# Performance work log

Measured on AMD Instinct MI355X. Metric: run time of the kernel, lower is better.

Reference implementation:

```python
import jax, jax.numpy as jnp
import numpy as np

N_NODES = 10240
N_EDGES = 40960
N_GRAPHS = 256
F_XD = 78
SEQ = 1000
VOCAB = 26
EMB = 128
NEG_SLOPE = 0.2


def gat_conv(x, src, dst, W, att_src, att_dst, bias, heads, f_out):
    """PyG GATConv (concat=True, self-loops, leaky_relu 0.2, dst-segment softmax)."""
    N = x.shape[0]
    h = (x @ W).reshape(N, heads, f_out)                      # [N,H,F]
    a_s = jnp.sum(h * att_src[None], axis=-1)                 # [N,H]
    a_d = jnp.sum(h * att_dst[None], axis=-1)                 # [N,H]
    loop = jnp.arange(N, dtype=src.dtype)
    s = jnp.concatenate([src, loop])                          # add self-loops
    d = jnp.concatenate([dst, loop])
    e = jax.nn.leaky_relu(a_s[s] + a_d[d], NEG_SLOPE)         # [E',H]
    m = jax.ops.segment_max(e, d, num_segments=N)             # stable softmax per dst
    e = jnp.exp(e - m[d])
    denom = jax.ops.segment_sum(e, d, num_segments=N)
    alpha = e / (denom[d] + 1e-16)                            # [E',H]
    out = jax.ops.segment_sum(alpha[:, :, None] * h[s], d, num_segments=N)
    return out.reshape(N, heads * f_out) + bias


def conv1d(x, w, b):
    y = jax.lax.conv_general_dilated(x, w, window_strides=(1,), padding='VALID',
                                     dimension_numbers=('NCH', 'OIH', 'NCH'))
    return y + b[None, :, None]


def maxpool1d(x, k):
    return jax.lax.reduce_window(x, -jnp.inf, jax.lax.max, (1, 1, k), (1, 1, k), 'VALID')


def setup_inputs() -> dict:
    key = jax.random.key(0)
    ks = jax.random.split(key, 32)
    x = jax.random.normal(ks[0], (N_NODES, F_XD), jnp.float32)
    src = jax.random.randint(ks[1], (N_EDGES,), 0, N_NODES, dtype=jnp.int32)
    dst = jax.random.randint(ks[2], (N_EDGES,), 0, N_NODES, dtype=jnp.int32)
    dst = jnp.where(dst == src, (dst + 1) % N_NODES, dst)     # no pre-existing self loops
    edge_index = jnp.stack([src, dst])
    batch = jnp.repeat(jnp.arange(N_GRAPHS, dtype=jnp.int32), N_NODES // N_GRAPHS)
    target = jax.random.randint(ks[3], (N_GRAPHS, SEQ), 0, VOCAB, dtype=jnp.int32)
    def w(k, shape):
        return jax.random.normal(k, shape, jnp.float32) * 0.05
    p = {
        'W1': w(ks[4], (78, 10 * 78)), 'as1': w(ks[5], (10, 78)), 'ad1': w(ks[6], (10, 78)), 'b1': jnp.zeros((780,), jnp.float32),
        'W2': w(ks[7], (780, 2 * 780)), 'as2': w(ks[8], (2, 780)), 'ad2': w(ks[9], (2, 780)), 'b2': jnp.zeros((1560,), jnp.float32),
        'W3': w(ks[10], (1560, 3120)), 'as3': w(ks[11], (1, 3120)), 'ad3': w(ks[12], (1, 3120)), 'b3': jnp.zeros((3120,), jnp.float32),
        'fc_g1_w': w(ks[13], (3120, 1024)), 'fc_g1_b': jnp.zeros((1024,), jnp.float32),
        'fc_g2_w': w(ks[14], (1024, 128)), 'fc_g2_b': jnp.zeros((128,), jnp.float32),
        'emb_xt': w(ks[15], (VOCAB, EMB)),
        'cw1': w(ks[16], (32, 1000, 8)), 'cb1': jnp.zeros((32,), jnp.float32),
        'cw2': w(ks[17], (64, 32, 8)), 'cb2': jnp.zeros((64,), jnp.float32),
        'cw3': w(ks[18], (96, 64, 8)), 'cb3': jnp.zeros((96,), jnp.float32),
        'cw4': w(ks[19], (128, 96, 8)), 'cb4': jnp.zeros((128,), jnp.float32),
        'fc1_xt_w': w(ks[20], (128 * 33, 1024)), 'fc1_xt_b': jnp.zeros((1024,), jnp.float32),
        'fc2_xt_w': w(ks[21], (1024, 128)), 'fc2_xt_b': jnp.zeros((128,), jnp.float32),
        'fc1_w': w(ks[22], (256, 1024)), 'fc1_b': jnp.zeros((1024,), jnp.float32),
        'fc2_w': w(ks[23], (1024, 256)), 'fc2_b': jnp.zeros((256,), jnp.float32),
        'out_w': w(ks[24], (256, 1)), 'out_b': jnp.zeros((1,), jnp.float32),
    }
    return {'x': x, 'edge_index': edge_index, 'batch': batch, 'target': target, **p}


def reference(x, edge_index, batch, target,
              W1, as1, ad1, b1, W2, as2, ad2, b2, W3, as3, ad3, b3,
              fc_g1_w, fc_g1_b, fc_g2_w, fc_g2_b, emb_xt,
              cw1, cb1, cw2, cb2, cw3, cb3, cw4, cb4,
              fc1_xt_w, fc1_xt_b, fc2_xt_w, fc2_xt_b,
              fc1_w, fc1_b, fc2_w, fc2_b, out_w, out_b):
    src, dst = edge_index[0], edge_index[1]
    # --- GAT branch (dropout layers are identity in eval mode) ---
    h = jax.nn.elu(gat_conv(x, src, dst, W1, as1, ad1, b1, 10, 78))
    h = jax.nn.relu(gat_conv(h, src, dst, W2, as2, ad2, b2, 2, 780))
    h = jax.nn.relu(gat_conv(h, src, dst, W3, as3, ad3, b3, 1, 3120))
    g = jax.ops.segment_max(h, batch, num_segments=N_GRAPHS)   # global max pool
    g = jax.nn.relu(g @ fc_g1_w + fc_g1_b)
    g = g @ fc_g2_w + fc_g2_b                                  # [B,128]
    # --- protein CNN branch ---
    e = emb_xt[target]                                         # [B,1000,128]
    c = jax.nn.relu(conv1d(e, cw1, cb1))                       # [B,32,121]
    c = jax.nn.relu(conv1d(c, cw2, cb2))                       # [B,64,114]
    c = jax.nn.relu(conv1d(c, cw3, cb3))                       # [B,96,107]
    c = jax.nn.relu(conv1d(c, cw4, cb4))                       # [B,128,100]
    c = maxpool1d(c, 3)                                        # [B,128,33]
    xt = c.reshape(N_GRAPHS, 128 * 33)
    xt = jax.nn.relu(xt @ fc1_xt_w + fc1_xt_b)
    xt = xt @ fc2_xt_w + fc2_xt_b                              # [B,128]
    # --- fusion head ---
    xc = jnp.concatenate([g, xt], axis=1)                      # [B,256]
    xc = jax.nn.relu(xc @ fc1_w + fc1_b)
    xc = jax.nn.relu(xc @ fc2_w + fc2_b)
    return xc @ out_w + out_b                                  # [B,1]
```

## Files before the change

### kernel.cpp

```cpp
#include <hip/hip_runtime.h>
#include <hip/hip_bf16.h>
#include <math.h>

static const int NNODES = 10240;
static const int NEDGES = 40960;
static const int NB     = 256;
static const int VOCAB  = 26;
static const int EMB    = 128;
static const int LP     = 128;
static const int C1SPLIT = 8;

typedef short bf16x8 __attribute__((ext_vector_type(8)));
typedef float f32x4  __attribute__((ext_vector_type(4)));

__device__ __forceinline__ float bf16bits2float(short s) {
    return __uint_as_float(((unsigned)(unsigned short)s) << 16);
}

__global__ __launch_bounds__(256) void gemm_f32_splitk_sl(
    const float* __restrict__ A, const float* __restrict__ B,
    float* __restrict__ P, int M, int N, int K, int kchunk)
{
    __shared__ float As[16][65];
    __shared__ float Bs[16][65];
    int tid = threadIdx.x;
    int bm = blockIdx.y * 64;
    int bn = blockIdx.x * 64;
    int z = blockIdx.z;
    int k0 = z * kchunk;
    int k1 = min(k0 + kchunk, K);
    int tx = tid & 15, ty = tid >> 4;
    float acc[4][4] = {};
    for (int kb = k0; kb < k1; kb += 16) {
#pragma unroll
        for (int l = 0; l < 4; ++l) {
            int idx = tid + l * 256;
            int r = idx >> 4, c = idx & 15;
            int gr = bm + r, gc = kb + c;
            As[c][r] = (gr < M && gc < k1) ? A[(size_t)gr * K + gc] : 0.f;
        }
#pragma unroll
        for (int l = 0; l < 4; ++l) {
            int idx = tid + l * 256;
            int r = idx >> 6, c = idx & 63;
            int gr = kb + r, gc = bn + c;
            Bs[r][c] = (gr < k1 && gc < N) ? B[(size_t)gr * N + gc] : 0.f;
        }
        __syncthreads();
#pragma unroll
        for (int kk = 0; kk < 16; ++kk) {
            float a[4], b[4];
#pragma unroll
            for (int i = 0; i < 4; ++i) a[i] = As[kk][ty * 4 + i];
#pragma unroll
            for (int j = 0; j < 4; ++j) b[j] = Bs[kk][tx * 4 + j];
#pragma unroll
            for (int i = 0; i < 4; ++i)
#pragma unroll
                for (int j = 0; j < 4; ++j)
                    acc[i][j] += a[i] * b[j];
        }
        __syncthreads();
    }
    float* Pz = P + (size_t)z * M * N;
#pragma unroll
    for (int i = 0; i < 4; ++i) {
        int gr = bm + ty * 4 + i;
        if (gr >= M) continue;
#pragma unroll
        for (int j = 0; j < 4; ++j) {
            int gc = bn + tx * 4 + j;
            if (gc >= N) continue;
            Pz[(size_t)gr * N + gc] = acc[i][j];
        }
    }
}

template<int ACT>
__global__ void reduce_bias_act_ld_kernel(const float* __restrict__ P,
                                          const float* __restrict__ bias,
                                          float* __restrict__ C,
                                          int M, int N, int S, int ldC)
{
    int t = blockIdx.x * 256 + threadIdx.x;
    if (t >= M * N) return;
    int r = t / N, c = t - r * N;
    float v = bias[c];
    for (int s = 0; s < S; ++s) v += P[(size_t)s * M * N + t];
    if (ACT == 1) v = fmaxf(v, 0.f);
    C[(size_t)r * ldC + c] = v;
}

__global__ void out_head_kernel(const float* __restrict__ f2,
                                const float* __restrict__ w,
                                const float* __restrict__ b,
                                float* __restrict__ out)
{
    __shared__ float sw[256];
    int t = threadIdx.x;
    sw[t] = w[t];
    __syncthreads();
    float acc = 0.f;
    const float* row = f2 + (size_t)t * 256;
    for (int k = 0; k < 256; ++k) acc += row[k] * sw[k];
    out[t] = acc + b[0];
}

__global__ void cast_a_kernel(const float* __restrict__ in, __hip_bfloat16* __restrict__ out,
                              int M, int K, int Kp)
{
    int idx = blockIdx.x * 256 + threadIdx.x;
    if (idx >= M * Kp) return;
    int r = idx / Kp, k = idx - r * Kp;
    out[idx] = __float2bfloat16(k < K ? in[(size_t)r * K + k] : 0.f);
}

__global__ __launch_bounds__(256) void transpose_cast_kernel(
    const float* __restrict__ in, __hip_bfloat16* __restrict__ out,
    int K, int N, int Kp, int Npad)
{
    __shared__ float tile[32][33];
    int k0 = blockIdx.x * 32;
    int n0 = blockIdx.y * 32;
    int tx = threadIdx.x & 31;
    int ty = threadIdx.x >> 5;
#pragma unroll
    for (int j = 0; j < 4; ++j) {
        int k = k0 + ty + j * 8, n = n0 + tx;
        tile[ty + j * 8][tx] = (k < K && n < N) ? in[(size_t)k * N + n] : 0.f;
    }
    __syncthreads();
#pragma unroll
    for (int j = 0; j < 4; ++j) {
        int n = n0 + ty + j * 8, k = k0 + tx;
        if (n < Npad && k < Kp)
            out[(size_t)n * Kp + k] = __float2bfloat16(tile[tx][ty + j * 8]);
    }
}

__global__ void conv_wt_all_kernel(
    const float* __restrict__ cw2, const float* __restrict__ cw3,
    const float* __restrict__ cw4, const float* __restrict__ cw1,
    __hip_bfloat16* __restrict__ wt2, __hip_bfloat16* __restrict__ wt3,
    __hip_bfloat16* __restrict__ wt4, float* __restrict__ wt1f)
{
    int idx = blockIdx.x * 256 + threadIdx.x;
    const int n2 = 64 * 32 * 8, n3 = 96 * 64 * 8, n4 = 128 * 96 * 8;
    if (idx < n2) {
        int o = idx / (32 * 8), rem = idx - o * 32 * 8;
        int i = rem >> 3, k = rem & 7;
        wt2[(size_t)o * 256 + k * 32 + i] = __float2bfloat16(cw2[idx]);
    } else if (idx < n2 + n3) {
        int j = idx - n2;
        int o = j / (64 * 8), rem = j - o * 64 * 8;
        int i = rem >> 3, k = rem & 7;
        wt3[(size_t)o * 512 + k * 64 + i] = __float2bfloat16(cw3[j]);
    } else if (idx < n2 + n3 + n4) {
        int j = idx - n2 - n3;
        int o = j / (96 * 8), rem = j - o * 96 * 8;
        int i = rem >> 3, k = rem & 7;
        wt4[(size_t)o * 768 + k * 96 + i] = __float2bfloat16(cw4[j]);
    } else {
        int j = idx - n2 - n3 - n4;
        if (j >= 32 * 8000) return;
        int o = j / 8000, rem = j - o * 8000;
        int i = rem >> 3, k = rem & 7;
        wt1f[(size_t)i * 256 + o * 8 + k] = cw1[j];
    }
}

__device__ __forceinline__ void stage_tile(
    const __hip_bfloat16* __restrict__ gA, int ldA,
    const __hip_bfloat16* __restrict__ gB, int ldB,
    short* ldsbuf, int w, int l)
{
#pragma unroll
    for (int j = 0; j < 4; ++j) {
        int u = (w * 4 + j) * 64 + l;
        int r = u >> 3, s = u & 7;
        const __hip_bfloat16* src = gA + (size_t)r * ldA + ((s ^ (r & 7)) << 3);
        __builtin_amdgcn_global_load_lds(
            (const __attribute__((address_space(1))) void*)src,
            (__attribute__((address_space(3))) void*)(ldsbuf + (w * 4 + j) * 512),
            16, 0, 0);
    }
#pragma unroll
    for (int j = 0; j < 4; ++j) {
        int u = (w * 4 + j) * 64 + l;
        int r = u >> 3, s = u & 7;
        const __hip_bfloat16* src = gB + (size_t)r * ldB + ((s ^ (r & 7)) << 3);
        __builtin_amdgcn_global_load_lds(
            (const __attribute__((address_space(1))) void*)src,
            (__attribute__((address_space(3))) void*)(ldsbuf + 8192 + (w * 4 + j) * 512),
            16, 0, 0);
    }
}

__global__ __launch_bounds__(256, 2) void gemm_mfma_bf16(
    const __hip_bfloat16* __restrict__ A,
    const __hip_bfloat16* __restrict__ Bt,
    __hip_bfloat16* __restrict__ C, int M, int N, int Kp, int ldC)
{
    __shared__ __align__(16) short lds[2][16384];
    const int tid = threadIdx.x;
    const int w = tid >> 6, l = tid & 63;

    int nwg = gridDim.x * gridDim.y;
    int wg = blockIdx.y * gridDim.x + blockIdx.x;
    int q = nwg >> 3, r8 = nwg & 7;
    int xcd = wg & 7, lo = wg >> 3;
    int swz = (xcd < r8) ? (xcd * (q + 1) + lo) : (r8 * (q + 1) + (xcd - r8) * q + lo);
    const int bm = (swz / gridDim.x) * 128, bn = (swz % gridDim.x) * 128;

    const int wr = w >> 1, wc = w & 1;
    const int lane15 = l & 15, lhi = l >> 4;

    const __hip_bfloat16* gA = A + (size_t)bm * Kp;
    const __hip_bfloat16* gB = Bt + (size_t)bn * Kp;

    f32x4 acc[4][4] = {};

    const int nk = Kp >> 6;
    stage_tile(gA, Kp, gB, Kp, &lds[0][0], w, l);
    __syncthreads();
    int cur = 0;
    for (int t = 0; t < nk; ++t) {
        if (t + 1 < nk)
            stage_tile(gA + (t + 1) * 64, Kp, gB + (t + 1) * 64, Kp, &lds[cur ^ 1][0], w, l);
        const short* bA = &lds[cur][0];
        const short* bB = &lds[cur][8192];
#pragma unroll
        for (int ks = 0; ks < 2; ++ks) {
            bf16x8 af[4], bfr[4];
#pragma unroll
            for (int m = 0; m < 4; ++m) {
                int r = wr * 64 + m * 16 + lane15;
                int slot = (ks * 4 + lhi) ^ (r & 7);
                af[m] = *(const bf16x8*)(bA + r * 64 + slot * 8);
            }
#pragma unroll
            for (int n = 0; n < 4; ++n) {
                int r = wc * 64 + n * 16 + lane15;
                int slot = (ks * 4 + lhi) ^ (r & 7);
                bfr[n] = *(const bf16x8*)(bB + r * 64 + slot * 8);
            }
#pragma unroll
            for (int m = 0; m < 4; ++m)
#pragma unroll
                for (int n = 0; n < 4; ++n)
                    acc[m][n] = __builtin_amdgcn_mfma_f32_16x16x32_bf16(
                        af[m], bfr[n], acc[m][n], 0, 0, 0);
        }
        __syncthreads();
        cur ^= 1;
    }
#pragma unroll
    for (int m = 0; m < 4; ++m) {
#pragma unroll
        for (int n = 0; n < 4; ++n) {
            int col = bn + wc * 64 + n * 16 + lane15;
            if (col >= N) continue;
            int row0 = bm + wr * 64 + m * 16 + lhi * 4;
#pragma unroll
            for (int q2 = 0; q2 < 4; ++q2)
                C[(size_t)(row0 + q2) * ldC + col] = __float2bfloat16(acc[m][n][q2]);
        }
    }
}

__global__ __launch_bounds__(256, 2) void gemm_mfma_splitk(
    const __hip_bfloat16* __restrict__ A,
    const __hip_bfloat16* __restrict__ Bt,
    float* __restrict__ P, int M, int N, int Kp, int tps)
{
    __shared__ __align__(16) short lds[2][16384];
    const int tid = threadIdx.x;
    const int w = tid >> 6, l = tid & 63;
    const int bm = blockIdx.y * 128, bn = blockIdx.x * 128;
    const int z = blockIdx.z;
    const int wr = w >> 1, wc = w & 1;
    const int lane15 = l & 15, lhi = l >> 4;

    const __hip_bfloat16* gA = A + (size_t)bm * Kp + z * tps * 64;
    const __hip_bfloat16* gB = Bt + (size_t)bn * Kp + z * tps * 64;

    f32x4 acc[4][4] = {};

    const int nk = tps;
    stage_tile(gA, Kp, gB, Kp, &lds[0][0], w, l);
    __syncthreads();
    int cur = 0;
    for (int t = 0; t < nk; ++t) {
        if (t + 1 < nk)
            stage_tile(gA + (t + 1) * 64, Kp, gB + (t + 1) * 64, Kp, &lds[cur ^ 1][0], w, l);
        const short* bA = &lds[cur][0];
        const short* bB = &lds[cur][8192];
#pragma unroll
        for (int ks = 0; ks < 2; ++ks) {
            bf16x8 af[4], bfr[4];
#pragma unroll
            for (int m = 0; m < 4; ++m) {
                int r = wr * 64 + m * 16 + lane15;
                int slot = (ks * 4 + lhi) ^ (r & 7);
                af[m] = *(const bf16x8*)(bA + r * 64 + slot * 8);
            }
#pragma unroll
            for (int n = 0; n < 4; ++n) {
                int r = wc * 64 + n * 16 + lane15;
                int slot = (ks * 4 + lhi) ^ (r & 7);
                bfr[n] = *(const bf16x8*)(bB + r * 64 + slot * 8);
            }
#pragma unroll
            for (int m = 0; m < 4; ++m)
#pragma unroll
                for (int n = 0; n < 4; ++n)
                    acc[m][n] = __builtin_amdgcn_mfma_f32_16x16x32_bf16(
                        af[m], bfr[n], acc[m][n], 0, 0, 0);
        }
        __syncthreads();
        cur ^= 1;
    }
    float* Pz = P + (size_t)z * M * N;
#pragma unroll
    for (int m = 0; m < 4; ++m) {
#pragma unroll
        for (int n = 0; n < 4; ++n) {
            int col = bn + wc * 64 + n * 16 + lane15;
            if (col >= N) continue;
            int row0 = bm + wr * 64 + m * 16 + lhi * 4;
#pragma unroll
            for (int q2 = 0; q2 < 4; ++q2) {
                int row = row0 + q2;
                if (row < M) Pz[(size_t)row * N + col] = acc[m][n][q2];
            }
        }
    }
}

template<int Ci, int Co, int Lout>
__global__ __launch_bounds__(256, 2) void gemm_conv_bf16(
    const __hip_bfloat16* __restrict__ A,
    const __hip_bfloat16* __restrict__ Bt,
    const float* __restrict__ bias,
    __hip_bfloat16* __restrict__ C)
{
    const int Kp = 8 * Ci;
    __shared__ __align__(16) short lds[2][16384];
    const int tid = threadIdx.x;
    const int w = tid >> 6, l = tid & 63;
    const int bm = blockIdx.y * 128;
    const int wr = w >> 1, wc = w & 1;
    const int lane15 = l & 15, lhi = l >> 4;

    const __hip_bfloat16* gA = A + (size_t)bm * Ci;
    const __hip_bfloat16* gB = Bt;

    f32x4 acc[4][4] = {};

    const int nk = Kp >> 6;
    stage_tile(gA, Ci, gB, Kp, &lds[0][0], w, l);
    __syncthreads();
    int cur = 0;
    for (int t = 0; t < nk; ++t) {
        if (t + 1 < nk)
            stage_tile(gA + (t + 1) * 64, Ci, gB + (t + 1) * 64, Kp, &lds[cur ^ 1][0], w, l);
        const short* bA = &lds[cur][0];
        const short* bB = &lds[cur][8192];
#pragma unroll
        for (int ks = 0; ks < 2; ++ks) {
            bf16x8 af[4], bfr[4];
#pragma unroll
            for (int m = 0; m < 4; ++m) {
                int r = wr * 64 + m * 16 + lane15;
                int slot = (ks * 4 + lhi) ^ (r & 7);
                af[m] = *(const bf16x8*)(bA + r * 64 + slot * 8);
            }
#pragma unroll
            for (int n = 0; n < 4; ++n) {
                int r = wc * 64 + n * 16 + lane15;
                int slot = (ks * 4 + lhi) ^ (r & 7);
                bfr[n] = *(const bf16x8*)(bB + r * 64 + slot * 8);
            }
#pragma unroll
            for (int m = 0; m < 4; ++m)
#pragma unroll
                for (int n = 0; n < 4; ++n)
                    acc[m][n] = __builtin_amdgcn_mfma_f32_16x16x32_bf16(
                        af[m], bfr[n], acc[m][n], 0, 0, 0);
        }
        __syncthreads();
        cur ^= 1;
    }
#pragma unroll
    for (int m = 0; m < 4; ++m) {
#pragma unroll
        for (int n = 0; n < 4; ++n) {
            int col = wc * 64 + n * 16 + lane15;
            if (col >= Co) continue;
            float bb = bias[col];
            int lr0 = wr * 64 + m * 16 + lhi * 4;
#pragma unroll
            for (int q2 = 0; q2 < 4; ++q2) {
                int lr = lr0 + q2;
                if (lr < Lout)
                    C[((size_t)bm + lr) * Co + col] =
                        __float2bfloat16(fmaxf(acc[m][n][q2] + bb, 0.f));
            }
        }
    }
}

__global__ __launch_bounds__(256, 2) void gemm_conv4_pool_bf16(
    const __hip_bfloat16* __restrict__ A,
    const __hip_bfloat16* __restrict__ Bt,
    const float* __restrict__ bias,
    __hip_bfloat16* __restrict__ xtb)
{
    const int Ci = 96, Kp = 768;
    __shared__ __align__(16) short lds[2][16384];
    const int tid = threadIdx.x;
    const int w = tid >> 6, l = tid & 63;
    const int bm = blockIdx.y * 128;
    const int wr = w >> 1, wc = w & 1;
    const int lane15 = l & 15, lhi = l >> 4;

    const __hip_bfloat16* gA = A + (size_t)bm * Ci;
    const __hip_bfloat16* gB = Bt;

    f32x4 acc[4][4] = {};

    const int nk = Kp >> 6;
    stage_tile(gA, Ci, gB, Kp, &lds[0][0], w, l);
    __syncthreads();
    int cur = 0;
    for (int t = 0; t < nk; ++t) {
        if (t + 1 < nk)
            stage_tile(gA + (t + 1) * 64, Ci, gB + (t + 1) * 64, Kp, &lds[cur ^ 1][0], w, l);
        const short* bA = &lds[cur][0];
        const short* bB = &lds[cur][8192];
#pragma unroll
        for (int ks = 0; ks < 2; ++ks) {
            bf16x8 af[4], bfr[4];
#pragma unroll
            for (int m = 0; m < 4; ++m) {
                int r = wr * 64 + m * 16 + lane15;
                int slot = (ks * 4 + lhi) ^ (r & 7);
                af[m] = *(const bf16x8*)(bA + r * 64 + slot * 8);
            }
#pragma unroll
            for (int n = 0; n < 4; ++n) {
                int r = wc * 64 + n * 16 + lane15;
                int slot = (ks * 4 + lhi) ^ (r & 7);
                bfr[n] = *(const bf16x8*)(bB + r * 64 + slot * 8);
            }
#pragma unroll
            for (int m = 0; m < 4; ++m)
#pragma unroll
                for (int n = 0; n < 4; ++n)
                    acc[m][n] = __builtin_amdgcn_mfma_f32_16x16x32_bf16(
                        af[m], bfr[n], acc[m][n], 0, 0, 0);
        }
        __syncthreads();
        cur ^= 1;
    }
    float* pbuf = (float*)&lds[0][0];
#pragma unroll
    for (int m = 0; m < 4; ++m) {
#pragma unroll
        for (int n = 0; n < 4; ++n) {
            int col = wc * 64 + n * 16 + lane15;
            float bb = bias[col];
            int lr0 = wr * 64 + m * 16 + lhi * 4;
#pragma unroll
            for (int q2 = 0; q2 < 4; ++q2)
                pbuf[(lr0 + q2) * 128 + col] = acc[m][n][q2] + bb;
        }
    }
    __syncthreads();
    int nb = blockIdx.y;
    for (int idx = tid; idx < 4352; idx += 256) {
        __hip_bfloat16 v;
        if (idx >= 4224) {
            v = __float2bfloat16(0.f);
        } else {
            int c = idx / 33, tp = idx - c * 33;
            float m3 = fmaxf(fmaxf(pbuf[(tp * 3) * 128 + c], pbuf[(tp * 3 + 1) * 128 + c]),
                             pbuf[(tp * 3 + 2) * 128 + c]);
            v = __float2bfloat16(fmaxf(m3, 0.f));
        }
        xtb[(size_t)nb * 4352 + idx] = v;
    }
}

__device__ __forceinline__ unsigned fmap(float f) {
    unsigned u = __float_as_uint(f);
    return (u & 0x80000000u) ? ~u : (u | 0x80000000u);
}
__device__ __forceinline__ float funmap(unsigned u) {
    return (u & 0x80000000u) ? __uint_as_float(u ^ 0x80000000u)
                             : __uint_as_float(~u);
}

__global__ void attn_ab_kernel(const __hip_bfloat16* __restrict__ lin, int Ftp,
                               const float* __restrict__ att_s,
                               const float* __restrict__ att_d,
                               float* __restrict__ a_s, float* __restrict__ a_d,
                               int H, int F)
{
    int bid = blockIdx.x;
    int n = bid / H, h = bid - n * H;
    int lane = threadIdx.x;
    const __hip_bfloat16* row = lin + (size_t)n * Ftp + h * F;
    const float* wsrc = att_s + h * F;
    const float* wdst = att_d + h * F;
    float ss = 0.f, sd = 0.f;
    for (int f = lane; f < F; f += 64) {
        float v = __bfloat162float(row[f]);
        ss += v * wsrc[f];
        sd += v * wdst[f];
    }
    for (int o = 32; o; o >>= 1) {
        ss += __shfl_down(ss, o);
        sd += __shfl_down(sd, o);
    }
    if (lane == 0) { a_s[bid] = ss; a_d[bid] = sd; }
}

__global__ void edge_max_kernel(const int* __restrict__ ei,
                                const float* __restrict__ a_s,
                                const float* __restrict__ a_d,
                                float* __restrict__ eval,
                                unsigned* __restrict__ mmax,
                                int E, int Etot, int H)
{
    int t = blockIdx.x * blockDim.x + threadIdx.x;
    if (t >= Etot * H) return;
    int e = t / H, h = t - e * H;
    int s, d;
    if (e < E) { s = ei[e]; d = ei[E + e]; } else { s = d = e - E; }
    float v = a_s[s * H + h] + a_d[d * H + h];
    v = v > 0.f ? v : 0.2f * v;
    eval[t] = v;
    atomicMax(&mmax[d * H + h], fmap(v));
}

__global__ void edge_exp_kernel(const int* __restrict__ ei,
                                const unsigned* __restrict__ mmax,
                                float* __restrict__ eval,
                                float* __restrict__ denom,
                                int E, int Etot, int H)
{
    int t = blockIdx.x * blockDim.x + threadIdx.x;
    if (t >= Etot * H) return;
    int e = t / H, h = t - e * H;
    int d = (e < E) ? ei[E + e] : e - E;
    float m = funmap(mmax[d * H + h]);
    float ex = expf(eval[t] - m);
    eval[t] = ex;
    atomicAdd(&denom[d * H + h], ex);
}

__global__ void deg_kernel(const int* __restrict__ ei, int* __restrict__ deg,
                           int E, int Etot)
{
    int e = blockIdx.x * 256 + threadIdx.x;
    if (e >= Etot) return;
    int d = (e < E) ? ei[E + e] : e - E;
    atomicAdd(&deg[d], 1);
}

__global__ __launch_bounds__(256) void scan_kernel(const int* __restrict__ deg,
                                                   int* __restrict__ rowptr,
                                                   int* __restrict__ cursor, int n)
{
    __shared__ int partial[256];
    int tid = threadIdx.x;
    const int per = (n + 255) / 256;
    int base = tid * per;
    int sum = 0;
    for (int i = 0; i < per; ++i) {
        int idx = base + i;
        if (idx < n) sum += deg[idx];
    }
    partial[tid] = sum;
    __syncthreads();
    for (int offs = 1; offs < 256; offs <<= 1) {
        int v = (tid >= offs) ? partial[tid - offs] : 0;
        __syncthreads();
        partial[tid] += v;
        __syncthreads();
    }
    int run = (tid == 0) ? 0 : partial[tid - 1];
    for (int i = 0; i < per; ++i) {
        int idx = base + i;
        if (idx < n) { rowptr[idx] = run; cursor[idx] = run; run += deg[idx]; }
    }
    if (tid == 255) rowptr[n] = run;
}

__global__ void fill_csr_kernel(const int* __restrict__ ei, int* __restrict__ cursor,
                                int* __restrict__ eidx, int E, int Etot)
{
    int e = blockIdx.x * 256 + threadIdx.x;
    if (e >= Etot) return;
    int d = (e < E) ? ei[E + e] : e - E;
    int pos = atomicAdd(&cursor[d], 1);
    eidx[pos] = e;
}

template<int ACT>
__global__ __launch_bounds__(64) void gat_gather8_kernel(
    const int* __restrict__ rowptr, const int* __restrict__ eidx,
    const int* __restrict__ ei, const float* __restrict__ eval,
    const float* __restrict__ denom,
    const __hip_bfloat16* __restrict__ lin, int Ftp,
    const float* __restrict__ bias,
    __hip_bfloat16* __restrict__ outh, int Kout,
    int E, int H, int F, int Ft)
{
    int d = blockIdx.x;
    int g = blockIdx.y * 64 + threadIdx.x;
    int c0 = g * 8;
    if (c0 >= Kout) return;
    bf16x8 res;
    if (c0 >= Ft) {
#pragma unroll
        for (int j = 0; j < 8; ++j) res[j] = 0;
        *(bf16x8*)(outh + (size_t)d * Kout + c0) = res;
        return;
    }
    int hj[8];
    float rdh[8];
#pragma unroll
    for (int j = 0; j < 8; ++j) {
        hj[j] = min((c0 + j) / F, H - 1);
        rdh[j] = 1.f / (denom[d * H + hj[j]] + 1e-16f);
    }
    float acc[8] = {};
    int p0 = rowptr[d], p1 = rowptr[d + 1];
    for (int p = p0; p < p1; ++p) {
        int e = eidx[p];
        int s = (e < E) ? ei[e] : e - E;
        bf16x8 v = *(const bf16x8*)(lin + (size_t)s * Ftp + c0);
        const float* aE = eval + (size_t)e * H;
        if (H == 1) {
            float a = aE[0] * rdh[0];
#pragma unroll
            for (int j = 0; j < 8; ++j)
                acc[j] += a * bf16bits2float(v[j]);
        } else {
#pragma unroll
            for (int j = 0; j < 8; ++j)
                acc[j] += aE[hj[j]] * rdh[j] * bf16bits2float(v[j]);
        }
    }
#pragma unroll
    for (int j = 0; j < 8; ++j) {
        int c = c0 + j;
        float val = 0.f;
        if (c < Ft) {
            val = acc[j] + bias[c];
            if (ACT == 1) val = fmaxf(val, 0.f);
            else if (ACT == 2) val = val > 0.f ? val : expm1f(val);
        }
        __hip_bfloat16 bv = __float2bfloat16(val);
        res[j] = *(const short*)&bv;
    }
    *(bf16x8*)(outh + (size_t)d * Kout + c0) = res;
}

__global__ void pool_max_bf16_kernel(const __hip_bfloat16* __restrict__ h,
                                     __hip_bfloat16* __restrict__ g,
                                     int B, int per, int C, int Kout)
{
    int t = blockIdx.x * blockDim.x + threadIdx.x;
    if (t >= B * Kout) return;
    int b = t / Kout, f = t - b * Kout;
    if (f >= C) { g[t] = __float2bfloat16(0.f); return; }
    const __hip_bfloat16* p = h + (size_t)b * per * C + f;
    float m = -INFINITY;
    for (int j = 0; j < per; ++j) m = fmaxf(m, __bfloat162float(p[(size_t)j * C]));
    g[t] = __float2bfloat16(m);
}

__global__ __launch_bounds__(256) void conv1_p1_kernel(
    const int* __restrict__ target, const float* __restrict__ wt,
    float* __restrict__ Spart)
{
    __shared__ float s_S[VOCAB * 256];
    __shared__ int   s_trow[125];
    int tid = threadIdx.x;
    int n = blockIdx.x, z = blockIdx.y;
    for (int i = tid; i < VOCAB * 256; i += 256) s_S[i] = 0.f;
    if (tid < 125) s_trow[tid] = target[n * 1000 + z * 125 + tid];
    __syncthreads();
    const float* wz = wt + (size_t)(z * 125) * 256 + tid;
    for (int i = 0; i < 125; ++i) {
        int v = s_trow[i];
        s_S[v * 256 + tid] += wz[(size_t)i * 256];
    }
    __syncthreads();
    float* outp = Spart + ((size_t)n * C1SPLIT + z) * (VOCAB * 256);
    for (int i = tid; i < VOCAB * 256; i += 256) outp[i] = s_S[i];
}

__global__ __launch_bounds__(256) void conv1_p2_kernel(
    const float* __restrict__ Spart, const float* __restrict__ emb,
    const float* __restrict__ b, __hip_bfloat16* __restrict__ y)
{
    __shared__ float s_emb[VOCAB * EMB];
    __shared__ float s_S[VOCAB * 256];
    int tid = threadIdx.x;
    int n = blockIdx.x;
    for (int i = tid; i < VOCAB * EMB; i += 256) s_emb[i] = emb[i];
    const float* base = Spart + (size_t)n * C1SPLIT * (VOCAB * 256);
    for (int i = tid; i < VOCAB * 256; i += 256) {
        float s = 0.f;
#pragma unroll
        for (int z = 0; z < C1SPLIT; ++z) s += base[(size_t)z * (VOCAB * 256) + i];
        s_S[i] = s;
    }
    __syncthreads();
    for (int idx = tid; idx < 121 * 32; idx += 256) {
        int t = idx >> 5, o = idx & 31;
        float acc = b[o];
#pragma unroll
        for (int v = 0; v < VOCAB; ++v) {
            const float* Sv = s_S + v * 256 + o * 8;
            const float* ev = s_emb + v * EMB + t;
#pragma unroll
            for (int k = 0; k < 8; ++k) acc += Sv[k] * ev[k];
        }
        y[((size_t)n * LP + t) * 32 + o] = __float2bfloat16(fmaxf(acc, 0.f));
    }
}

extern "C" void kernel_launch(void* const* d_in, const int* in_sizes, int n_in,
                              void* d_out, int out_size, void* d_ws, size_t ws_size,
                              hipStream_t stream)
{
    const float* x      = (const float*)d_in[0];
    const int*   ei     = (const int*)d_in[1];
    const int*   target = (const int*)d_in[3];
    const float* W1  = (const float*)d_in[4];
    const float* as1 = (const float*)d_in[5];
    const float* ad1 = (const float*)d_in[6];
    const float* b1  = (const float*)d_in[7];
    const float* W2  = (const float*)d_in[8];
    const float* as2 = (const float*)d_in[9];
    const float* ad2 = (const float*)d_in[10];
    const float* b2  = (const float*)d_in[11];
    const float* W3  = (const float*)d_in[12];
    const float* as3 = (const float*)d_in[13];
    const float* ad3 = (const float*)d_in[14];
    const float* b3  = (const float*)d_in[15];
    const float* fc_g1_w = (const float*)d_in[16];
    const float* fc_g1_b = (const float*)d_in[17];
    const float* fc_g2_w = (const float*)d_in[18];
    const float* fc_g2_b = (const float*)d_in[19];
    const float* emb_xt  = (const float*)d_in[20];
    const float* cw1 = (const float*)d_in[21];
    const float* cb1 = (const float*)d_in[22];
    const float* cw2 = (const float*)d_in[23];
    const float* cb2 = (const float*)d_in[24];
    const float* cw3 = (const float*)d_in[25];
    const float* cb3 = (const float*)d_in[26];
    const float* cw4 = (const float*)d_in[27];
    const float* cb4 = (const float*)d_in[28];
    const float* fc1_xt_w = (const float*)d_in[29];
    const float* fc1_xt_b = (const float*)d_in[30];
    const float* fc2_xt_w = (const float*)d_in[31];
    const float* fc2_xt_b = (const float*)d_in[32];
    const float* fc1_w = (const float*)d_in[33];
    const float* fc1_b = (const float*)d_in[34];
    const float* fc2_w = (const float*)d_in[35];
    const float* fc2_b = (const float*)d_in[36];
    const float* out_w = (const float*)d_in[37];
    const float* out_b = (const float*)d_in[38];
    float* out = (float*)d_out;

    const int N = NNODES, E = NEDGES, Etot = E + N;
    const size_t MB = 1024 * 1024;

    char* ws = (char*)d_ws;
    size_t off = 0;
    auto alloc = [&](size_t bytes) -> char* {
        char* p = ws + off;
        off = (off + bytes + 255) & ~(size_t)255;
        return p;
    };
    const size_t BIG = (size_t)N * 3120 * sizeof(float);
    char*  bufA  = alloc(BIG);
    char*  bufB  = alloc(BIG);
    float*    a_s   = (float*)alloc((size_t)N * 10 * 4);
    float*    a_d   = (float*)alloc((size_t)N * 10 * 4);
    char*     mmdn  = alloc((size_t)2 * N * 10 * 4);
    float*    eval  = (float*)alloc((size_t)Etot * 10 * 4);
    float*    g1    = (float*)alloc((size_t)NB * 1024 * 4);
    float*    xt1   = (float*)alloc((size_t)NB * 1024 * 4);
    float*    xc    = (float*)alloc((size_t)NB * 256 * 4);
    float*    f1    = (float*)alloc((size_t)NB * 1024 * 4);
    float*    f2    = (float*)alloc((size_t)NB * 256 * 4);
    __hip_bfloat16* gbufb = (__hip_bfloat16*)alloc((size_t)NB * 3200 * 2);
    __hip_bfloat16* xtb   = (__hip_bfloat16*)alloc((size_t)NB * 4352 * 2);
    int*      deg     = (int*)alloc((size_t)N * 4);
    int*      rowptr  = (int*)alloc((size_t)(N + 1) * 4);
    int*      cursor  = (int*)alloc((size_t)N * 4);
    int*      eidx    = (int*)alloc((size_t)Etot * 4);

    __hip_bfloat16* linb = (__hip_bfloat16*)bufA;
    __hip_bfloat16* Wt   = (__hip_bfloat16*)(bufA + 64 * MB);
    __hip_bfloat16* xb   = (__hip_bfloat16*)(bufA + 80 * MB);
    __hip_bfloat16* hbf1 = (__hip_bfloat16*)bufB;
    __hip_bfloat16* hbf2 = (__hip_bfloat16*)(bufB + 20 * MB);
    __hip_bfloat16* hbf3 = (__hip_bfloat16*)bufB;
    __hip_bfloat16* Wt2  = (__hip_bfloat16*)(bufB + 105 * MB);
    float*          P4   = (float*)(bufB + 115 * MB);

    char* cnn = bufA;
    auto calloc2 = [&](size_t bytes) -> char* {
        char* p = cnn;
        cnn += (bytes + 255) & ~(size_t)255;
        return p;
    };
    __hip_bfloat16* act1 = (__hip_bfloat16*)calloc2((size_t)NB * LP * 32 * 2 + 4096);
    __hip_bfloat16* act2 = (__hip_bfloat16*)calloc2((size_t)NB * LP * 64 * 2 + 4096);
    __hip_bfloat16* act3 = (__hip_bfloat16*)calloc2((size_t)NB * LP * 96 * 2 + 4096);
    __hip_bfloat16* wt2  = (__hip_bfloat16*)calloc2((size_t)128 * 256 * 2);
    __hip_bfloat16* wt3  = (__hip_bfloat16*)calloc2((size_t)128 * 512 * 2);
    __hip_bfloat16* wt4  = (__hip_bfloat16*)calloc2((size_t)128 * 768 * 2);
    float* wt1f  = (float*)calloc2((size_t)1000 * 256 * 4);
    float* Spart = (float*)calloc2((size_t)NB * C1SPLIT * VOCAB * 256 * 4);

    {
        (void)hipMemsetAsync(deg, 0, (size_t)N * 4, stream);
        deg_kernel<<<(Etot + 255) / 256, 256, 0, stream>>>(ei, deg, E, Etot);
        scan_kernel<<<1, 256, 0, stream>>>(deg, rowptr, cursor, N);
        fill_csr_kernel<<<(Etot + 255) / 256, 256, 0, stream>>>(ei, cursor, eidx, E, Etot);
    }

    auto head_gemm = [&](const float* A, const float* B, const float* bias, float* C,
                         int M, int Nc, int K, int ldC, int act, int S) {
        int kchunk = (K + S - 1) / S;
        dim3 g((Nc + 63) / 64, (M + 63) / 64, S);
        gemm_f32_splitk_sl<<<g, 256, 0, stream>>>(A, B, P4, M, Nc, K, kchunk);
        int tot = M * Nc;
        if (act == 1)
            reduce_bias_act_ld_kernel<1><<<(tot + 255) / 256, 256, 0, stream>>>(P4, bias, C, M, Nc, S, ldC);
        else
            reduce_bias_act_ld_kernel<0><<<(tot + 255) / 256, 256, 0, stream>>>(P4, bias, C, M, Nc, S, ldC);
    };

    auto head_gemm_mfma = [&](const __hip_bfloat16* Ab_, const float* W, const float* bias,
                              float* C, int M, int Nc, int K, int Kp, int S) {
        int tps = (Kp / 64) / S;
        transpose_cast_kernel<<<dim3(Kp / 32, Nc / 32), 256, 0, stream>>>(W, Wt2, K, Nc, Kp, Nc);
        dim3 g(Nc / 128, M / 128, S);
        gemm_mfma_splitk<<<g, 256, 0, stream>>>(Ab_, Wt2, P4, M, Nc, Kp, tps);
        int tot = M * Nc;
        reduce_bias_act_ld_kernel<1><<<(tot + 255) / 256, 256, 0, stream>>>(P4, bias, C, M, Nc, S, Nc);
    };

    auto gat_tail = [&](const float* atts, const float* attd, const float* bias,
                        int H, int F, int Ftp, int act,
                        const __hip_bfloat16* lin, __hip_bfloat16* outh, int Kout) {
        unsigned* mmax = (unsigned*)mmdn;
        float* denom = (float*)(mmdn + (size_t)N * H * 4);
        attn_ab_kernel<<<N * H, 64, 0, stream>>>(lin, Ftp, atts, attd, a_s, a_d, H, F);
        (void)hipMemsetAsync(mmdn, 0, (size_t)2 * N * H * 4, stream);
        int tot = Etot * H;
        edge_max_kernel<<<(tot + 255) / 256, 256, 0, stream>>>(ei, a_s, a_d, eval, mmax, E, Etot, H);
        edge_exp_kernel<<<(tot + 255) / 256, 256, 0, stream>>>(ei, mmax, eval, denom, E, Etot, H);
        int Ft = H * F;
        int groups = Kout / 8;
        dim3 gg(N, (groups + 63) / 64);
        if (act == 1)
            gat_gather8_kernel<1><<<gg, 64, 0, stream>>>(rowptr, eidx, ei, eval, denom, lin, Ftp, bias, outh, Kout, E, H, F, Ft);
        else
            gat_gather8_kernel<2><<<gg, 64, 0, stream>>>(rowptr, eidx, ei, eval, denom, lin, Ftp, bias, outh, Kout, E, H, F, Ft);
    };

    {
        (void)hipMemsetAsync(linb, 0, (size_t)N * 784 * 2, stream);
        cast_a_kernel<<<(N * 128 + 255) / 256, 256, 0, stream>>>(x, xb, N, 78, 128);
        transpose_cast_kernel<<<dim3(4, 28), 256, 0, stream>>>(W1, Wt, 78, 780, 128, 896);
        gemm_mfma_bf16<<<dim3(7, N / 128), 256, 0, stream>>>(xb, Wt, linb, N, 780, 128, 784);
        gat_tail(as1, ad1, b1, 10, 78, 784, 2, linb, hbf1, 832);
    }
    {
        const int Kp = 832, Nout = 1560, Npad = 1664;
        transpose_cast_kernel<<<dim3(Kp / 32, Npad / 32), 256, 0, stream>>>(W2, Wt, 780, Nout, Kp, Npad);
        gemm_mfma_bf16<<<dim3(Npad / 128, N / 128), 256, 0, stream>>>(hbf1, Wt, linb, N, Nout, Kp, Nout);
        gat_tail(as2, ad2, b2, 2, 780, 1560, 1, linb, hbf2, 1600);
    }
    {
        const int Kp = 1600, Nout = 3120, Npad = 3200;
        transpose_cast_kernel<<<dim3(Kp / 32, Npad / 32), 256, 0, stream>>>(W3, Wt, 1560, Nout, Kp, Npad);
        gemm_mfma_bf16<<<dim3(Npad / 128, N / 128), 256, 0, stream>>>(hbf2, Wt, linb, N, Nout, Kp, Nout);
        gat_tail(as3, ad3, b3, 1, 3120, 3120, 1, linb, hbf3, 3120);
    }

    {
        int tot = NB * 3200;
        pool_max_bf16_kernel<<<(tot + 255) / 256, 256, 0, stream>>>(hbf3, gbufb, NB, N / NB, 3120, 3200);
        head_gemm_mfma(gbufb, fc_g1_w, fc_g1_b, g1, NB, 1024, 3120, 3200, 5);
        head_gemm(g1, fc_g2_w, fc_g2_b, xc, NB, 128, 1024, 256, 0, 32);
    }

    {
        conv_wt_all_kernel<<<(64 * 32 * 8 + 96 * 64 * 8 + 128 * 96 * 8 + 32 * 8000 + 255) / 256,
                             256, 0, stream>>>(cw2, cw3, cw4, cw1, wt2, wt3, wt4, wt1f);
        conv1_p1_kernel<<<dim3(NB, C1SPLIT), 256, 0, stream>>>(target, wt1f, Spart);
        conv1_p2_kernel<<<NB, 256, 0, stream>>>(Spart, emb_xt, cb1, act1);
        gemm_conv_bf16<32, 64, 114><<<dim3(1, NB), 256, 0, stream>>>(act1, wt2, cb2, act2);
        gemm_conv_bf16<64, 96, 107><<<dim3(1, NB), 256, 0, stream>>>(act2, wt3, cb3, act3);
        gemm_conv4_pool_bf16<<<dim3(1, NB), 256, 0, stream>>>(act3, wt4, cb4, xtb);
        head_gemm_mfma(xtb, fc1_xt_w, fc1_xt_b, xt1, NB, 1024, 4224, 4352, 4);
        head_gemm(xt1, fc2_xt_w, fc2_xt_b, xc + 128, NB, 128, 1024, 256, 0, 32);
    }

    {
        head_gemm(xc, fc1_w, fc1_b, f1, NB, 1024, 256, 1024, 1, 8);
        head_gemm(f1, fc2_w, fc2_b, f2, NB, 256, 1024, 256, 1, 16);
        out_head_kernel<<<1, 256, 0, stream>>>(f2, out_w, out_b, out);
    }
}
```

Baseline: 793.5 us.

## Fuse GAT edge softmax into CSR gather kernel, dropping atomic max/sum passes

Removes the separate edge_max and edge_exp kernels, the memset and the eval/denominator buffers. Each gather thread now recomputes the leaky-relu attention logits for its destination's incoming edges, takes the per-head max in a first pass, then computes the exp weights, their sum and the weighted feature accumulation in a second pass, normalising at the end. This removes atomics and several launches per layer. In exchange, every column-group thread recomputes the softmax terms redundantly and walks the edge list twice.

```diff
diff --git a/kernel.cpp b/kernel.cpp
--- a/kernel.cpp
+++ b/kernel.cpp
@@ -492,15 +492,6 @@
     }
 }
 
-__device__ __forceinline__ unsigned fmap(float f) {
-    unsigned u = __float_as_uint(f);
-    return (u & 0x80000000u) ? ~u : (u | 0x80000000u);
-}
-__device__ __forceinline__ float funmap(unsigned u) {
-    return (u & 0x80000000u) ? __uint_as_float(u ^ 0x80000000u)
-                             : __uint_as_float(~u);
-}
-
 __global__ void attn_ab_kernel(const __hip_bfloat16* __restrict__ lin, int Ftp,
                                const float* __restrict__ att_s,
                                const float* __restrict__ att_d,
@@ -526,40 +517,6 @@
     if (lane == 0) { a_s[bid] = ss; a_d[bid] = sd; }
 }
 
-__global__ void edge_max_kernel(const int* __restrict__ ei,
-                                const float* __restrict__ a_s,
-                                const float* __restrict__ a_d,
-                                float* __restrict__ eval,
-                                unsigned* __restrict__ mmax,
-                                int E, int Etot, int H)
-{
-    int t = blockIdx.x * blockDim.x + threadIdx.x;
-    if (t >= Etot * H) return;
-    int e = t / H, h = t - e * H;
-    int s, d;
-    if (e < E) { s = ei[e]; d = ei[E + e]; } else { s = d = e - E; }
-    float v = a_s[s * H + h] + a_d[d * H + h];
-    v = v > 0.f ? v : 0.2f * v;
-    eval[t] = v;
-    atomicMax(&mmax[d * H + h], fmap(v));
-}
-
-__global__ void edge_exp_kernel(const int* __restrict__ ei,
-                                const unsigned* __restrict__ mmax,
-                                float* __restrict__ eval,
-                                float* __restrict__ denom,
-                                int E, int Etot, int H)
-{
-    int t = blockIdx.x * blockDim.x + threadIdx.x;
-    if (t >= Etot * H) return;
-    int e = t / H, h = t - e * H;
-    int d = (e < E) ? ei[E + e] : e - E;
-    float m = funmap(mmax[d * H + h]);
-    float ex = expf(eval[t] - m);
-    eval[t] = ex;
-    atomicAdd(&denom[d * H + h], ex);
-}
-
 __global__ void deg_kernel(const int* __restrict__ ei, int* __restrict__ deg,
                            int E, int Etot)
 {
@@ -611,8 +568,8 @@
 template<int ACT>
 __global__ __launch_bounds__(64) void gat_gather8_kernel(
     const int* __restrict__ rowptr, const int* __restrict__ eidx,
-    const int* __restrict__ ei, const float* __restrict__ eval,
-    const float* __restrict__ denom,
+    const int* __restrict__ ei,
+    const float* __restrict__ a_s, const float* __restrict__ a_d,
     const __hip_bfloat16* __restrict__ lin, int Ftp,
     const float* __restrict__ bias,
     __hip_bfloat16* __restrict__ outh, int Kout,
@@ -629,37 +586,62 @@
         *(bf16x8*)(outh + (size_t)d * Kout + c0) = res;
         return;
     }
-    int hj[8];
-    float rdh[8];
-#pragma unroll
-    for (int j = 0; j < 8; ++j) {
-        hj[j] = min((c0 + j) / F, H - 1);
-        rdh[j] = 1.f / (denom[d * H + hj[j]] + 1e-16f);
-    }
-    float acc[8] = {};
+    int h0 = min(c0 / F, H - 1);
+    int h1 = min((c0 + 7) / F, H - 1);
+    int split = (h1 == h0) ? 8 : (F * (h0 + 1) - c0);
+    float ad0 = a_d[d * H + h0];
+    float ad1 = (h1 == h0) ? ad0 : a_d[d * H + h1];
     int p0 = rowptr[d], p1 = rowptr[d + 1];
+
+    float m0 = -INFINITY, m1 = -INFINITY;
     for (int p = p0; p < p1; ++p) {
         int e = eidx[p];
         int s = (e < E) ? ei[e] : e - E;
+        float v0 = a_s[s * H + h0] + ad0;
+        v0 = v0 > 0.f ? v0 : 0.2f * v0;
+        m0 = fmaxf(m0, v0);
+        if (h1 != h0) {
+            float v1 = a_s[s * H + h1] + ad1;
+            v1 = v1 > 0.f ? v1 : 0.2f * v1;
+            m1 = fmaxf(m1, v1);
+        }
+    }
+    if (h1 == h0) m1 = m0;
+
+    float acc[8] = {};
+    float sum0 = 0.f, sum1 = 0.f;
+    for (int p = p0; p < p1; ++p) {
+        int e = eidx[p];
+        int s = (e < E) ? ei[e] : e - E;
+        float v0 = a_s[s * H + h0] + ad0;
+        v0 = v0 > 0.f ? v0 : 0.2f * v0;
+        float w0 = expf(v0 - m0);
+        sum0 += w0;
+        float w1;
+        if (h1 != h0) {
+            float v1 = a_s[s * H + h1] + ad1;
+            v1 = v1 > 0.f ? v1 : 0.2f * v1;
+            w1 = expf(v1 - m1);
+            sum1 += w1;
+        } else {
+            w1 = w0;
+        }
         bf16x8 v = *(const bf16x8*)(lin + (size_t)s * Ftp + c0);
-        const float* aE = eval + (size_t)e * H;
-        if (H == 1) {
-            float a = aE[0] * rdh[0];
-#pragma unroll
-            for (int j = 0; j < 8; ++j)
-                acc[j] += a * bf16bits2float(v[j]);
-        } else {
-#pragma unroll
-            for (int j = 0; j < 8; ++j)
-                acc[j] += aE[hj[j]] * rdh[j] * bf16bits2float(v[j]);
-        }
-    }
+#pragma unroll
+        for (int j = 0; j < 8; ++j) {
+            float wv = (j < split) ? w0 : w1;
+            acc[j] += wv * bf16bits2float(v[j]);
+        }
+    }
+    float rs0 = 1.f / (sum0 + 1e-16f);
+    float rs1 = (h1 == h0) ? rs0 : 1.f / (sum1 + 1e-16f);
+
 #pragma unroll
     for (int j = 0; j < 8; ++j) {
         int c = c0 + j;
         float val = 0.f;
         if (c < Ft) {
-            val = acc[j] + bias[c];
+            val = acc[j] * ((j < split) ? rs0 : rs1) + bias[c];
             if (ACT == 1) val = fmaxf(val, 0.f);
             else if (ACT == 2) val = val > 0.f ? val : expm1f(val);
         }
@@ -794,8 +776,6 @@
     char*  bufB  = alloc(BIG);
     float*    a_s   = (float*)alloc((size_t)N * 10 * 4);
     float*    a_d   = (float*)alloc((size_t)N * 10 * 4);
-    char*     mmdn  = alloc((size_t)2 * N * 10 * 4);
-    float*    eval  = (float*)alloc((size_t)Etot * 10 * 4);
     float*    g1    = (float*)alloc((size_t)NB * 1024 * 4);
     float*    xt1   = (float*)alloc((size_t)NB * 1024 * 4);
     float*    xc    = (float*)alloc((size_t)NB * 256 * 4);
@@ -864,20 +844,14 @@
     auto gat_tail = [&](const float* atts, const float* attd, const float* bias,
                         int H, int F, int Ftp, int act,
                         const __hip_bfloat16* lin, __hip_bfloat16* outh, int Kout) {
-        unsigned* mmax = (unsigned*)mmdn;
-        float* denom = (float*)(mmdn + (size_t)N * H * 4);
         attn_ab_kernel<<<N * H, 64, 0, stream>>>(lin, Ftp, atts, attd, a_s, a_d, H, F);
-        (void)hipMemsetAsync(mmdn, 0, (size_t)2 * N * H * 4, stream);
-        int tot = Etot * H;
-        edge_max_kernel<<<(tot + 255) / 256, 256, 0, stream>>>(ei, a_s, a_d, eval, mmax, E, Etot, H);
-        edge_exp_kernel<<<(tot + 255) / 256, 256, 0, stream>>>(ei, mmax, eval, denom, E, Etot, H);
         int Ft = H * F;
         int groups = Kout / 8;
         dim3 gg(N, (groups + 63) / 64);
         if (act == 1)
-            gat_gather8_kernel<1><<<gg, 64, 0, stream>>>(rowptr, eidx, ei, eval, denom, lin, Ftp, bias, outh, Kout, E, H, F, Ft);
+            gat_gather8_kernel<1><<<gg, 64, 0, stream>>>(rowptr, eidx, ei, a_s, a_d, lin, Ftp, bias, outh, Kout, E, H, F, Ft);
         else
-            gat_gather8_kernel<2><<<gg, 64, 0, stream>>>(rowptr, eidx, ei, eval, denom, lin, Ftp, bias, outh, Kout, E, H, F, Ft);
+            gat_gather8_kernel<2><<<gg, 64, 0, stream>>>(rowptr, eidx, ei, a_s, a_d, lin, Ftp, bias, outh, Kout, E, H, F, Ft);
     };
 
     {
```

Result: faster. 759.9 us (-4.2%).
